# Kernel tuning notes

Hardware: AMD Instinct MI355X
Metric: run time of the kernel (lower is better)

Reference implementation:

```python
import jax, jax.numpy as jnp
import numpy as np

N_NODES = 50000
N_EDGES = 800000
N_CEDGES = 200000
D = 128


def setup_inputs() -> dict:
    key = jax.random.key(0)
    ks = jax.random.split(key, 8)
    return {
        "node_attr": jax.random.normal(ks[0], (N_NODES, D), jnp.float32),
        "edge_attr": jax.random.normal(ks[1], (N_EDGES, D), jnp.float32),
        "edge_contact_attr": jax.random.normal(ks[2], (N_CEDGES, D), jnp.float32),
        "receivers_idx": jax.random.randint(ks[3], (N_EDGES,), 0, N_NODES),
        "receivers_contact_idx": jax.random.randint(ks[4], (N_CEDGES,), 0, N_NODES),
        "W1": jax.random.normal(ks[5], (3 * D, D), jnp.float32) * (1.0 / np.sqrt(3 * D)),
        "b1": jnp.zeros((D,), jnp.float32),
        "W2": jax.random.normal(ks[6], (D, D), jnp.float32) * (1.0 / np.sqrt(D)),
        "b2": jnp.zeros((D,), jnp.float32),
        "ln_gamma": jnp.ones((D,), jnp.float32),
        "ln_beta": jnp.zeros((D,), jnp.float32),
    }


def _scatter_mean(vals, idx, num_segments):
    # scatter_mean semantics: mean over contributions; 0 for empty segments
    sums = jax.ops.segment_sum(vals, idx, num_segments=num_segments)  # [N, D]
    cnt = jax.ops.segment_sum(jnp.ones((vals.shape[0],), vals.dtype), idx,
                              num_segments=num_segments)  # [N]
    return sums / jnp.maximum(cnt, 1.0)[:, None]


def _layer_norm(x, gamma, beta, eps=1e-5):
    mu = jnp.mean(x, axis=-1, keepdims=True)
    var = jnp.var(x, axis=-1, keepdims=True)
    return (x - mu) * jax.lax.rsqrt(var + eps) * gamma + beta


def reference(node_attr, edge_attr, edge_contact_attr, receivers_idx,
              receivers_contact_idx, W1, b1, W2, b2, ln_gamma, ln_beta):
    n = node_attr.shape[0]
    agg_mesh = _scatter_mean(edge_attr, receivers_idx, n)                 # [N, D]
    agg_contact = _scatter_mean(edge_contact_attr, receivers_contact_idx, n)  # [N, D]
    concat = jnp.concatenate([node_attr, agg_mesh, agg_contact], axis=-1)  # [N, 3D]
    h = jax.nn.relu(concat @ W1 + b1)
    h = h @ W2 + b2
    new_node_attr = _layer_norm(h, ln_gamma, ln_beta)
    return new_node_attr
```

## Files before the change

### kernel.cpp

```cpp
#include <hip/hip_runtime.h>

#define N_NODES 50000
#define N_EDGES 800000
#define N_CEDGES 200000
#define D 128
#define CAP_M 128
#define CAP_C 64

typedef short s16x4 __attribute__((ext_vector_type(4)));
typedef short s16x8 __attribute__((ext_vector_type(8)));
typedef float f32x4 __attribute__((ext_vector_type(4)));
typedef __bf16 bf16x8 __attribute__((ext_vector_type(8)));
typedef int i32x4 __attribute__((ext_vector_type(4)));

__device__ __forceinline__ unsigned short f2bf(float f) {
    unsigned int u = __builtin_bit_cast(unsigned int, f);
    u = u + 0x7fffu + ((u >> 16) & 1u);
    return (unsigned short)(u >> 16);
}

__global__ void fill_pack_kernel(const int* __restrict__ rm, const int* __restrict__ rc,
                                 int* __restrict__ cnt_m, int* __restrict__ cnt_c,
                                 int* __restrict__ csr_m, int* __restrict__ csr_c,
                                 const float* __restrict__ W1, const float* __restrict__ W2,
                                 s16x8* __restrict__ wp1, s16x8* __restrict__ wp2) {
    if (blockIdx.x < 977) {
        int t = blockIdx.x * blockDim.x + threadIdx.x;
        if (t < N_EDGES / 4) {
            i32x4 r = *(const i32x4*)(rm + t * 4);
#pragma unroll
            for (int j = 0; j < 4; ++j) {
                int pos = atomicAdd(&cnt_m[r[j]], 1);
                if (pos < CAP_M) csr_m[r[j] * CAP_M + pos] = t * 4 + j;
            }
        } else if (t < N_EDGES / 4 + N_CEDGES / 4) {
            int t2 = t - N_EDGES / 4;
            i32x4 r = *(const i32x4*)(rc + t2 * 4);
#pragma unroll
            for (int j = 0; j < 4; ++j) {
                int pos = atomicAdd(&cnt_c[r[j]], 1);
                if (pos < CAP_C) csr_c[r[j] * CAP_C + pos] = t2 * 4 + j;
            }
        }
    } else {
        int t = (blockIdx.x - 977) * blockDim.x + threadIdx.x;
        if (t < 12 * 8 * 64) {
            int ks = t >> 9, rem = t & 511, nt = rem >> 6, l = rem & 63;
            int kb = ks * 32 + ((l >> 4) * 8), col = nt * 16 + (l & 15);
            s16x8 v;
#pragma unroll
            for (int j = 0; j < 8; ++j) v[j] = (short)f2bf(W1[(size_t)(kb + j) * D + col]);
            wp1[t] = v;
        } else if (t < (12 + 4) * 8 * 64) {
            int t2 = t - 12 * 8 * 64;
            int ks = t2 >> 9, rem = t2 & 511, nt = rem >> 6, l = rem & 63;
            int kb = ks * 32 + ((l >> 4) * 8), col = nt * 16 + (l & 15);
            s16x8 v;
#pragma unroll
            for (int j = 0; j < 8; ++j) v[j] = (short)f2bf(W2[(size_t)(kb + j) * D + col]);
            wp2[t2] = v;
        }
    }
}

__launch_bounds__(256)
__global__ void gather_kernel(const float* __restrict__ edge_attr,
                              const float* __restrict__ cedge_attr,
                              const int* __restrict__ csr_m, const int* __restrict__ csr_c,
                              const int* __restrict__ cnt_m, const int* __restrict__ cnt_c,
                              unsigned short* __restrict__ aggm, unsigned short* __restrict__ aggc) {
    const int lane = threadIdx.x & 63;
    const int n = blockIdx.x * 4 + (threadIdx.x >> 6);
    if (n >= N_NODES) return;
    const int q = lane >> 4;
    const int sub = lane & 15;
    const int c0 = sub * 8;

    {
        const int cnt = cnt_m[n];
        const int cm = cnt < CAP_M ? cnt : CAP_M;
        const int s = n * CAP_M;
        f32x4 a0 = (f32x4)0.f, a1 = (f32x4)0.f, b0 = (f32x4)0.f, b1 = (f32x4)0.f;
        for (int base = 0; base < cm; base += 64) {
            int m = cm - base; if (m > 64) m = 64;
            int idx = csr_m[s + base + (lane < m ? lane : m - 1)];
            int i = 0;
            for (; i + 8 <= m; i += 8) {
                int e0 = __shfl(idx, i + q);
                int e1 = __shfl(idx, i + 4 + q);
                const float* p0 = edge_attr + (size_t)e0 * D + c0;
                const float* p1 = edge_attr + (size_t)e1 * D + c0;
                f32x4 r0a = __builtin_nontemporal_load((const f32x4*)p0);
                f32x4 r0b = __builtin_nontemporal_load((const f32x4*)(p0 + 4));
                f32x4 r1a = __builtin_nontemporal_load((const f32x4*)p1);
                f32x4 r1b = __builtin_nontemporal_load((const f32x4*)(p1 + 4));
                a0 += r0a; b0 += r0b; a1 += r1a; b1 += r1b;
            }
            for (; i < m; i += 4) {
                int j = i + q;
                int e = __shfl(idx, j < m ? j : m - 1);
                if (j < m) {
                    const float* p = edge_attr + (size_t)e * D + c0;
                    f32x4 ra = __builtin_nontemporal_load((const f32x4*)p);
                    f32x4 rb = __builtin_nontemporal_load((const f32x4*)(p + 4));
                    a0 += ra; b0 += rb;
                }
            }
        }
        f32x4 alo = a0 + a1, ahi = b0 + b1;
#pragma unroll
        for (int k = 0; k < 4; ++k) {
            alo[k] += __shfl_xor(alo[k], 16); ahi[k] += __shfl_xor(ahi[k], 16);
            alo[k] += __shfl_xor(alo[k], 32); ahi[k] += __shfl_xor(ahi[k], 32);
        }
        const float inv = 1.0f / fmaxf((float)cnt, 1.0f);
        if (lane < 16) {
            s16x8 pv;
#pragma unroll
            for (int k = 0; k < 4; ++k) {
                pv[k]     = (short)f2bf(alo[k] * inv);
                pv[k + 4] = (short)f2bf(ahi[k] * inv);
            }
            *(s16x8*)(aggm + (size_t)n * D + c0) = pv;
        }
    }
    {
        const int cnt = cnt_c[n];
        const int cm = cnt < CAP_C ? cnt : CAP_C;
        const int s = n * CAP_C;
        f32x4 a0 = (f32x4)0.f, a1 = (f32x4)0.f, b0 = (f32x4)0.f, b1 = (f32x4)0.f;
        for (int base = 0; base < cm; base += 64) {
            int m = cm - base; if (m > 64) m = 64;
            int idx = csr_c[s + base + (lane < m ? lane : m - 1)];
            int i = 0;
            for (; i + 8 <= m; i += 8) {
                int e0 = __shfl(idx, i + q);
                int e1 = __shfl(idx, i + 4 + q);
                const float* p0 = cedge_attr + (size_t)e0 * D + c0;
                const float* p1 = cedge_attr + (size_t)e1 * D + c0;
                f32x4 r0a = __builtin_nontemporal_load((const f32x4*)p0);
                f32x4 r0b = __builtin_nontemporal_load((const f32x4*)(p0 + 4));
                f32x4 r1a = __builtin_nontemporal_load((const f32x4*)p1);
                f32x4 r1b = __builtin_nontemporal_load((const f32x4*)(p1 + 4));
                a0 += r0a; b0 += r0b; a1 += r1a; b1 += r1b;
            }
            for (; i < m; i += 4) {
                int j = i + q;
                int e = __shfl(idx, j < m ? j : m - 1);
                if (j < m) {
                    const float* p = cedge_attr + (size_t)e * D + c0;
                    f32x4 ra = __builtin_nontemporal_load((const f32x4*)p);
                    f32x4 rb = __builtin_nontemporal_load((const f32x4*)(p + 4));
                    a0 += ra; b0 += rb;
                }
            }
        }
        f32x4 alo = a0 + a1, ahi = b0 + b1;
#pragma unroll
        for (int k = 0; k < 4; ++k) {
            alo[k] += __shfl_xor(alo[k], 16); ahi[k] += __shfl_xor(ahi[k], 16);
            alo[k] += __shfl_xor(alo[k], 32); ahi[k] += __shfl_xor(ahi[k], 32);
        }
        const float inv = 1.0f / fmaxf((float)cnt, 1.0f);
        if (lane < 16) {
            s16x8 pv;
#pragma unroll
            for (int k = 0; k < 4; ++k) {
                pv[k]     = (short)f2bf(alo[k] * inv);
                pv[k + 4] = (short)f2bf(ahi[k] * inv);
            }
            *(s16x8*)(aggc + (size_t)n * D + c0) = pv;
        }
    }
}

__launch_bounds__(256, 3)
__global__ void gemm_fused_kernel(const float* __restrict__ node_attr,
                                  const unsigned short* __restrict__ aggm,
                                  const unsigned short* __restrict__ aggc,
                                  const s16x8* __restrict__ wp1,
                                  const s16x8* __restrict__ wp2,
                                  const float* __restrict__ b1,
                                  const float* __restrict__ b2,
                                  const float* __restrict__ gamma,
                                  const float* __restrict__ beta,
                                  float* __restrict__ out) {
    __shared__ short Xl[64 * 392];
    short* Hl = Xl;
    const int tid = threadIdx.x;
    const int lane = tid & 63;
    const int w = tid >> 6;
    const int m0 = blockIdx.x * 64;

#pragma unroll
    for (int it = 0; it < 8; ++it) {
        int c = tid + it * 256;
        int row = c >> 5, c4 = c & 31;
        float4 v = make_float4(0.f, 0.f, 0.f, 0.f);
        if (m0 + row < N_NODES) v = *(const float4*)(node_attr + (size_t)(m0 + row) * D + c4 * 4);
        s16x4 sv;
        sv[0] = (short)f2bf(v.x); sv[1] = (short)f2bf(v.y);
        sv[2] = (short)f2bf(v.z); sv[3] = (short)f2bf(v.w);
        *(s16x4*)&Xl[row * 392 + c4 * 4] = sv;
    }
#pragma unroll
    for (int it = 0; it < 4; ++it) {
        int c = tid + it * 256;
        int row = c >> 4, c8 = c & 15;
        s16x8 vm = (s16x8)0, vc = (s16x8)0;
        if (m0 + row < N_NODES) {
            vm = *(const s16x8*)(aggm + (size_t)(m0 + row) * D + c8 * 8);
            vc = *(const s16x8*)(aggc + (size_t)(m0 + row) * D + c8 * 8);
        }
        *(s16x8*)&Xl[row * 392 + 128 + c8 * 8] = vm;
        *(s16x8*)&Xl[row * 392 + 256 + c8 * 8] = vc;
    }
    __syncthreads();

    const int rrow = w * 16 + (lane & 15);
    const int kg = (lane >> 4) * 8;

    f32x4 acc[8];
#pragma unroll
    for (int nt = 0; nt < 8; ++nt) acc[nt] = (f32x4)0.0f;
#pragma unroll
    for (int ks = 0; ks < 12; ++ks) {
        s16x8 a = *(const s16x8*)&Xl[rrow * 392 + ks * 32 + kg];
#pragma unroll
        for (int nt = 0; nt < 8; ++nt) {
            s16x8 b = wp1[(ks * 8 + nt) * 64 + lane];
            acc[nt] = __builtin_amdgcn_mfma_f32_16x16x32_bf16(
                __builtin_bit_cast(bf16x8, a), __builtin_bit_cast(bf16x8, b), acc[nt], 0, 0, 0);
        }
    }
    __syncthreads();

#pragma unroll
    for (int nt = 0; nt < 8; ++nt) {
        float bias = b1[nt * 16 + (lane & 15)];
#pragma unroll
        for (int j = 0; j < 4; ++j) {
            float v = fmaxf(acc[nt][j] + bias, 0.0f);
            int r = w * 16 + (lane >> 4) * 4 + j;
            Hl[r * 136 + nt * 16 + (lane & 15)] = (short)f2bf(v);
        }
    }
    f32x4 acc2[8];
#pragma unroll
    for (int nt = 0; nt < 8; ++nt) acc2[nt] = (f32x4)0.0f;
#pragma unroll
    for (int ks = 0; ks < 4; ++ks) {
        s16x8 a = *(const s16x8*)&Hl[rrow * 136 + ks * 32 + kg];
#pragma unroll
        for (int nt = 0; nt < 8; ++nt) {
            s16x8 b = wp2[(ks * 8 + nt) * 64 + lane];
            acc2[nt] = __builtin_amdgcn_mfma_f32_16x16x32_bf16(
                __builtin_bit_cast(bf16x8, a), __builtin_bit_cast(bf16x8, b), acc2[nt], 0, 0, 0);
        }
    }
    float g8[8], be8[8], b28[8];
#pragma unroll
    for (int nt = 0; nt < 8; ++nt) {
        int c = nt * 16 + (lane & 15);
        g8[nt] = gamma[c]; be8[nt] = beta[c]; b28[nt] = b2[c];
    }
#pragma unroll
    for (int j = 0; j < 4; ++j) {
        float vv[8];
        float s = 0.f, qq = 0.f;
#pragma unroll
        for (int nt = 0; nt < 8; ++nt) {
            float v = acc2[nt][j] + b28[nt];
            vv[nt] = v; s += v; qq += v * v;
        }
#pragma unroll
        for (int m = 1; m < 16; m <<= 1) {
            s += __shfl_xor(s, m);
            qq += __shfl_xor(qq, m);
        }
        float mu = s * (1.0f / D);
        float var = qq * (1.0f / D) - mu * mu;
        float rs = rsqrtf(var + 1e-5f);
        int r = m0 + w * 16 + (lane >> 4) * 4 + j;
        if (r < N_NODES) {
#pragma unroll
            for (int nt = 0; nt < 8; ++nt)
                out[(size_t)r * D + nt * 16 + (lane & 15)] = (vv[nt] - mu) * rs * g8[nt] + be8[nt];
        }
    }
}


extern "C" void kernel_launch(void* const* d_in, const int* in_sizes, int n_in,
                              void* d_out, int out_size, void* d_ws, size_t ws_size,
                              hipStream_t stream) {
    const float* node_attr  = (const float*)d_in[0];
    const float* edge_attr  = (const float*)d_in[1];
    const float* cedge_attr = (const float*)d_in[2];
    const int*   rm         = (const int*)d_in[3];
    const int*   rc         = (const int*)d_in[4];
    const float* W1         = (const float*)d_in[5];
    const float* b1         = (const float*)d_in[6];
    const float* W2         = (const float*)d_in[7];
    const float* b2         = (const float*)d_in[8];
    const float* gamma      = (const float*)d_in[9];
    const float* beta       = (const float*)d_in[10];
    float* out = (float*)d_out;

    char* ws = (char*)d_ws;
    int* cnt_m  = (int*)(ws + 0);
    int* cnt_c  = (int*)(ws + 200704);
    int* csr_m  = (int*)(ws + 401408);
    int* csr_c  = (int*)(ws + 26001408);
    s16x8* wp1  = (s16x8*)(ws + 38801408);
    s16x8* wp2  = (s16x8*)(ws + 38899712);
    unsigned short* aggm = (unsigned short*)(ws + 38932480);
    unsigned short* aggc = (unsigned short*)(ws + 51732480);

    hipMemsetAsync(ws, 0, 401408, stream);

    fill_pack_kernel<<<1009, 256, 0, stream>>>(rm, rc, cnt_m, cnt_c, csr_m, csr_c,
                                               W1, W2, wp1, wp2);
    gather_kernel<<<12500, 256, 0, stream>>>(edge_attr, cedge_attr, csr_m, csr_c,
                                             cnt_m, cnt_c, aggm, aggc);
    gemm_fused_kernel<<<782, 256, 0, stream>>>(node_attr, aggm, aggc,
                                               wp1, wp2, b1, b2, gamma, beta, out);
}
```

Measured before the change: 229.6 us.

## Fuse edge gather-mean into the GEMM kernel, dropping intermediate aggregate buffers

Removes the separate gather kernel and computes the mesh and contact scatter-means directly into shared memory inside the fused MLP kernel. Each wave processes 16 nodes serially, with half-wave lanes loading 4 floats each from two edges at a time. This eliminates the bf16 aggregate round trip through global memory and one launch. In exchange, gather parallelism drops to the GEMM kernel's occupancy, which is limited by shared memory, so memory latency may be less well hidden.

Measured after the change: 280.7 us. +22.3%, slower.

```diff
diff --git a/kernel.cpp b/kernel.cpp
--- a/kernel.cpp
+++ b/kernel.cpp
@@ -17,6 +17,10 @@
     unsigned int u = __builtin_bit_cast(unsigned int, f);
     u = u + 0x7fffu + ((u >> 16) & 1u);
     return (unsigned short)(u >> 16);
+}
+
+__device__ __forceinline__ f32x4 ntload(const float* p) {
+    return __builtin_nontemporal_load((const f32x4*)p);
 }
 
 __global__ void fill_pack_kernel(const int* __restrict__ rm, const int* __restrict__ rc,
@@ -63,134 +67,24 @@
     }
 }
 
-__launch_bounds__(256)
-__global__ void gather_kernel(const float* __restrict__ edge_attr,
-                              const float* __restrict__ cedge_attr,
-                              const int* __restrict__ csr_m, const int* __restrict__ csr_c,
-                              const int* __restrict__ cnt_m, const int* __restrict__ cnt_c,
-                              unsigned short* __restrict__ aggm, unsigned short* __restrict__ aggc) {
-    const int lane = threadIdx.x & 63;
-    const int n = blockIdx.x * 4 + (threadIdx.x >> 6);
-    if (n >= N_NODES) return;
-    const int q = lane >> 4;
-    const int sub = lane & 15;
-    const int c0 = sub * 8;
-
-    {
-        const int cnt = cnt_m[n];
-        const int cm = cnt < CAP_M ? cnt : CAP_M;
-        const int s = n * CAP_M;
-        f32x4 a0 = (f32x4)0.f, a1 = (f32x4)0.f, b0 = (f32x4)0.f, b1 = (f32x4)0.f;
-        for (int base = 0; base < cm; base += 64) {
-            int m = cm - base; if (m > 64) m = 64;
-            int idx = csr_m[s + base + (lane < m ? lane : m - 1)];
-            int i = 0;
-            for (; i + 8 <= m; i += 8) {
-                int e0 = __shfl(idx, i + q);
-                int e1 = __shfl(idx, i + 4 + q);
-                const float* p0 = edge_attr + (size_t)e0 * D + c0;
-                const float* p1 = edge_attr + (size_t)e1 * D + c0;
-                f32x4 r0a = __builtin_nontemporal_load((const f32x4*)p0);
-                f32x4 r0b = __builtin_nontemporal_load((const f32x4*)(p0 + 4));
-                f32x4 r1a = __builtin_nontemporal_load((const f32x4*)p1);
-                f32x4 r1b = __builtin_nontemporal_load((const f32x4*)(p1 + 4));
-                a0 += r0a; b0 += r0b; a1 += r1a; b1 += r1b;
-            }
-            for (; i < m; i += 4) {
-                int j = i + q;
-                int e = __shfl(idx, j < m ? j : m - 1);
-                if (j < m) {
-                    const float* p = edge_attr + (size_t)e * D + c0;
-                    f32x4 ra = __builtin_nontemporal_load((const f32x4*)p);
-                    f32x4 rb = __builtin_nontemporal_load((const f32x4*)(p + 4));
-                    a0 += ra; b0 += rb;
-                }
-            }
-        }
-        f32x4 alo = a0 + a1, ahi = b0 + b1;
-#pragma unroll
-        for (int k = 0; k < 4; ++k) {
-            alo[k] += __shfl_xor(alo[k], 16); ahi[k] += __shfl_xor(ahi[k], 16);
-            alo[k] += __shfl_xor(alo[k], 32); ahi[k] += __shfl_xor(ahi[k], 32);
-        }
-        const float inv = 1.0f / fmaxf((float)cnt, 1.0f);
-        if (lane < 16) {
-            s16x8 pv;
-#pragma unroll
-            for (int k = 0; k < 4; ++k) {
-                pv[k]     = (short)f2bf(alo[k] * inv);
-                pv[k + 4] = (short)f2bf(ahi[k] * inv);
-            }
-            *(s16x8*)(aggm + (size_t)n * D + c0) = pv;
-        }
-    }
-    {
-        const int cnt = cnt_c[n];
-        const int cm = cnt < CAP_C ? cnt : CAP_C;
-        const int s = n * CAP_C;
-        f32x4 a0 = (f32x4)0.f, a1 = (f32x4)0.f, b0 = (f32x4)0.f, b1 = (f32x4)0.f;
-        for (int base = 0; base < cm; base += 64) {
-            int m = cm - base; if (m > 64) m = 64;
-            int idx = csr_c[s + base + (lane < m ? lane : m - 1)];
-            int i = 0;
-            for (; i + 8 <= m; i += 8) {
-                int e0 = __shfl(idx, i + q);
-                int e1 = __shfl(idx, i + 4 + q);
-                const float* p0 = cedge_attr + (size_t)e0 * D + c0;
-                const float* p1 = cedge_attr + (size_t)e1 * D + c0;
-                f32x4 r0a = __builtin_nontemporal_load((const f32x4*)p0);
-                f32x4 r0b = __builtin_nontemporal_load((const f32x4*)(p0 + 4));
-                f32x4 r1a = __builtin_nontemporal_load((const f32x4*)p1);
-                f32x4 r1b = __builtin_nontemporal_load((const f32x4*)(p1 + 4));
-                a0 += r0a; b0 += r0b; a1 += r1a; b1 += r1b;
-            }
-            for (; i < m; i += 4) {
-                int j = i + q;
-                int e = __shfl(idx, j < m ? j : m - 1);
-                if (j < m) {
-                    const float* p = cedge_attr + (size_t)e * D + c0;
-                    f32x4 ra = __builtin_nontemporal_load((const f32x4*)p);
-                    f32x4 rb = __builtin_nontemporal_load((const f32x4*)(p + 4));
-                    a0 += ra; b0 += rb;
-                }
-            }
-        }
-        f32x4 alo = a0 + a1, ahi = b0 + b1;
-#pragma unroll
-        for (int k = 0; k < 4; ++k) {
-            alo[k] += __shfl_xor(alo[k], 16); ahi[k] += __shfl_xor(ahi[k], 16);
-            alo[k] += __shfl_xor(alo[k], 32); ahi[k] += __shfl_xor(ahi[k], 32);
-        }
-        const float inv = 1.0f / fmaxf((float)cnt, 1.0f);
-        if (lane < 16) {
-            s16x8 pv;
-#pragma unroll
-            for (int k = 0; k < 4; ++k) {
-                pv[k]     = (short)f2bf(alo[k] * inv);
-                pv[k + 4] = (short)f2bf(ahi[k] * inv);
-            }
-            *(s16x8*)(aggc + (size_t)n * D + c0) = pv;
-        }
-    }
-}
-
 __launch_bounds__(256, 3)
-__global__ void gemm_fused_kernel(const float* __restrict__ node_attr,
-                                  const unsigned short* __restrict__ aggm,
-                                  const unsigned short* __restrict__ aggc,
-                                  const s16x8* __restrict__ wp1,
-                                  const s16x8* __restrict__ wp2,
-                                  const float* __restrict__ b1,
-                                  const float* __restrict__ b2,
-                                  const float* __restrict__ gamma,
-                                  const float* __restrict__ beta,
-                                  float* __restrict__ out) {
+__global__ void fused_kernel(const float* __restrict__ node_attr,
+                             const float* __restrict__ edge_attr,
+                             const float* __restrict__ cedge_attr,
+                             const int* __restrict__ csr_m, const int* __restrict__ csr_c,
+                             const int* __restrict__ cnt_m, const int* __restrict__ cnt_c,
+                             const s16x8* __restrict__ wp1, const s16x8* __restrict__ wp2,
+                             const float* __restrict__ b1, const float* __restrict__ b2,
+                             const float* __restrict__ gamma, const float* __restrict__ beta,
+                             float* __restrict__ out) {
     __shared__ short Xl[64 * 392];
     short* Hl = Xl;
     const int tid = threadIdx.x;
     const int lane = tid & 63;
     const int w = tid >> 6;
     const int m0 = blockIdx.x * 64;
+    const int half = lane >> 5;
+    const int l31 = lane & 31;
 
 #pragma unroll
     for (int it = 0; it < 8; ++it) {
@@ -203,17 +97,96 @@
         sv[2] = (short)f2bf(v.z); sv[3] = (short)f2bf(v.w);
         *(s16x4*)&Xl[row * 392 + c4 * 4] = sv;
     }
-#pragma unroll
-    for (int it = 0; it < 4; ++it) {
-        int c = tid + it * 256;
-        int row = c >> 4, c8 = c & 15;
-        s16x8 vm = (s16x8)0, vc = (s16x8)0;
-        if (m0 + row < N_NODES) {
-            vm = *(const s16x8*)(aggm + (size_t)(m0 + row) * D + c8 * 8);
-            vc = *(const s16x8*)(aggc + (size_t)(m0 + row) * D + c8 * 8);
-        }
-        *(s16x8*)&Xl[row * 392 + 128 + c8 * 8] = vm;
-        *(s16x8*)&Xl[row * 392 + 256 + c8 * 8] = vc;
+
+    for (int i = 0; i < 16; ++i) {
+        const int lrow = w * 16 + i;
+        const int n = m0 + lrow;
+        if (n < N_NODES) {
+            {
+                const int cnt = cnt_m[n];
+                const int cm = cnt < CAP_M ? cnt : CAP_M;
+                const int s = n * CAP_M;
+                f32x4 A0 = (f32x4)0.f, A1 = (f32x4)0.f, A2 = (f32x4)0.f, A3 = (f32x4)0.f;
+                for (int base = 0; base < cm; base += 64) {
+                    int m = cm - base; if (m > 64) m = 64;
+                    int idx = csr_m[s + base + (lane < m ? lane : m - 1)];
+                    int i2 = 0;
+                    for (; i2 + 8 <= m; i2 += 8) {
+                        int e0 = __shfl(idx, i2 + half);
+                        int e1 = __shfl(idx, i2 + 2 + half);
+                        int e2 = __shfl(idx, i2 + 4 + half);
+                        int e3 = __shfl(idx, i2 + 6 + half);
+                        A0 += ntload(edge_attr + (size_t)e0 * D + l31 * 4);
+                        A1 += ntload(edge_attr + (size_t)e1 * D + l31 * 4);
+                        A2 += ntload(edge_attr + (size_t)e2 * D + l31 * 4);
+                        A3 += ntload(edge_attr + (size_t)e3 * D + l31 * 4);
+                    }
+                    for (; i2 + 4 <= m; i2 += 4) {
+                        int e0 = __shfl(idx, i2 + half);
+                        int e1 = __shfl(idx, i2 + 2 + half);
+                        A0 += ntload(edge_attr + (size_t)e0 * D + l31 * 4);
+                        A1 += ntload(edge_attr + (size_t)e1 * D + l31 * 4);
+                    }
+                    for (; i2 < m; i2 += 2) {
+                        int j = i2 + half;
+                        int e = __shfl(idx, j < m ? j : m - 1);
+                        if (j < m) A0 += ntload(edge_attr + (size_t)e * D + l31 * 4);
+                    }
+                }
+                f32x4 A = (A0 + A1) + (A2 + A3);
+#pragma unroll
+                for (int k = 0; k < 4; ++k) A[k] += __shfl_xor(A[k], 32);
+                const float inv = 1.0f / fmaxf((float)cnt, 1.0f);
+                if (lane < 32) {
+                    s16x4 pv;
+#pragma unroll
+                    for (int k = 0; k < 4; ++k) pv[k] = (short)f2bf(A[k] * inv);
+                    *(s16x4*)&Xl[lrow * 392 + 128 + l31 * 4] = pv;
+                }
+            }
+            {
+                const int cnt = cnt_c[n];
+                const int cm = cnt < CAP_C ? cnt : CAP_C;
+                const int s = n * CAP_C;
+                f32x4 A0 = (f32x4)0.f, A1 = (f32x4)0.f, A2 = (f32x4)0.f, A3 = (f32x4)0.f;
+                for (int base = 0; base < cm; base += 64) {
+                    int m = cm - base; if (m > 64) m = 64;
+                    int idx = csr_c[s + base + (lane < m ? lane : m - 1)];
+                    int i2 = 0;
+                    for (; i2 + 8 <= m; i2 += 8) {
+                        int e0 = __shfl(idx, i2 + half);
+                        int e1 = __shfl(idx, i2 + 2 + half);
+                        int e2 = __shfl(idx, i2 + 4 + half);
+                        int e3 = __shfl(idx, i2 + 6 + half);
+                        A0 += ntload(cedge_attr + (size_t)e0 * D + l31 * 4);
+                        A1 += ntload(cedge_attr + (size_t)e1 * D + l31 * 4);
+                        A2 += ntload(cedge_attr + (size_t)e2 * D + l31 * 4);
+                        A3 += ntload(cedge_attr + (size_t)e3 * D + l31 * 4);
+                    }
+                    for (; i2 + 4 <= m; i2 += 4) {
+                        int e0 = __shfl(idx, i2 + half);
+                        int e1 = __shfl(idx, i2 + 2 + half);
+                        A0 += ntload(cedge_attr + (size_t)e0 * D + l31 * 4);
+                        A1 += ntload(cedge_attr + (size_t)e1 * D + l31 * 4);
+                    }
+                    for (; i2 < m; i2 += 2) {
+                        int j = i2 + half;
+                        int e = __shfl(idx, j < m ? j : m - 1);
+                        if (j < m) A0 += ntload(cedge_attr + (size_t)e * D + l31 * 4);
+                    }
+                }
+                f32x4 A = (A0 + A1) + (A2 + A3);
+#pragma unroll
+                for (int k = 0; k < 4; ++k) A[k] += __shfl_xor(A[k], 32);
+                const float inv = 1.0f / fmaxf((float)cnt, 1.0f);
+                if (lane < 32) {
+                    s16x4 pv;
+#pragma unroll
+                    for (int k = 0; k < 4; ++k) pv[k] = (short)f2bf(A[k] * inv);
+                    *(s16x4*)&Xl[lrow * 392 + 256 + l31 * 4] = pv;
+                }
+            }
+        }
     }
     __syncthreads();
 
@@ -314,15 +287,12 @@
     int* csr_c  = (int*)(ws + 26001408);
     s16x8* wp1  = (s16x8*)(ws + 38801408);
     s16x8* wp2  = (s16x8*)(ws + 38899712);
-    unsigned short* aggm = (unsigned short*)(ws + 38932480);
-    unsigned short* aggc = (unsigned short*)(ws + 51732480);
 
     hipMemsetAsync(ws, 0, 401408, stream);
 
     fill_pack_kernel<<<1009, 256, 0, stream>>>(rm, rc, cnt_m, cnt_c, csr_m, csr_c,
                                                W1, W2, wp1, wp2);
-    gather_kernel<<<12500, 256, 0, stream>>>(edge_attr, cedge_attr, csr_m, csr_c,
-                                             cnt_m, cnt_c, aggm, aggc);
-    gemm_fused_kernel<<<782, 256, 0, stream>>>(node_attr, aggm, aggc,
-                                               wp1, wp2, b1, b2, gamma, beta, out);
-}
+    fused_kernel<<<782, 256, 0, stream>>>(node_attr, edge_attr, cedge_attr,
+                                          csr_m, csr_c, cnt_m, cnt_c,
+                                          wp1, wp2, b1, b2, gamma, beta, out);
+}
```
